# Optimization experiments

Hardware: AMD Instinct MI355X
Metric: run time of the kernel (lower is better)

Reference implementation:

```python
import jax, jax.numpy as jnp
import numpy as np

N, E, C, L, OUT = 50000, 600000, 128, 2, 64


def setup_inputs() -> dict:
    key = jax.random.key(0)
    ks = jax.random.split(key, 8)
    s = 1.0 / np.sqrt(C)
    return {
        "x": jax.random.normal(ks[0], (N, C), jnp.float32),
        "edge_index": jax.random.randint(ks[1], (2, E), 0, N, jnp.int64),
        "W_neigh": jax.random.normal(ks[2], (L, C, C), jnp.float32) * s,
        "W_root": jax.random.normal(ks[3], (L, C, C), jnp.float32) * s,
        "b_conv": jnp.zeros((L, C), jnp.float32),
        "ln_gamma": jnp.ones((L, C), jnp.float32),
        "ln_beta": jnp.zeros((L, C), jnp.float32),
        "W_head": jax.random.normal(ks[4], (OUT, C), jnp.float32) * s,
        "b_head": jnp.zeros((OUT,), jnp.float32),
        "num_seed": 1024,
    }


def _layernorm(h, g, b, eps=1e-5):
    mu = jnp.mean(h, axis=-1, keepdims=True)
    var = jnp.mean(jnp.square(h - mu), axis=-1, keepdims=True)
    return (h - mu) * jax.lax.rsqrt(var + eps) * g + b


def reference(x, edge_index, W_neigh, W_root, b_conv, ln_gamma, ln_beta, W_head, b_head, num_seed):
    src, dst = edge_index[0], edge_index[1]
    n = x.shape[0]
    # in-degree for mean aggregation (clamped to 1 as in PyG mean aggr)
    deg = jax.ops.segment_sum(jnp.ones((src.shape[0],), x.dtype), dst, num_segments=n)
    inv_deg = 1.0 / jnp.maximum(deg, 1.0)  # [N]
    for l in range(W_neigh.shape[0]):
        agg = jax.ops.segment_sum(x[src], dst, num_segments=n) * inv_deg[:, None]  # [N,C]
        h = agg @ W_neigh[l].T + x @ W_root[l].T + b_conv[l]
        x = jax.nn.relu(_layernorm(h, ln_gamma[l], ln_beta[l]))
    # head on the seed nodes (entity table slice starts at 0 here)
    return x[:num_seed] @ W_head.T + b_head
```

## Files before the change

### kernel.cpp

```cpp
#include <hip/hip_runtime.h>

#define C 128

typedef __attribute__((ext_vector_type(8))) short short8;
typedef __attribute__((ext_vector_type(16))) float floatx16;

__device__ __forceinline__ unsigned short f2b(float f) {
    union { float f; unsigned u; } v; v.f = f;
    unsigned u = v.u + 0x7fffu + ((v.u >> 16) & 1u);
    return (unsigned short)(u >> 16);
}
__device__ __forceinline__ float b2f(unsigned short h) {
    union { unsigned u; float f; } v; v.u = ((unsigned)h) << 16;
    return v.f;
}
__device__ __forceinline__ void acc_pair(unsigned u, float& lo, float& hi) {
    union { unsigned u; float f; } a, b;
    a.u = u << 16;
    b.u = u & 0xffff0000u;
    lo += a.f;
    hi += b.f;
}

__global__ void mark_kernel(const int* __restrict__ src, const int* __restrict__ dst,
                            int* __restrict__ needed, int E, int num_seed) {
    int t = blockIdx.x * blockDim.x + threadIdx.x;
    if (t < num_seed) needed[t] = 1;
    if (t < E) {
        int d = dst[t];
        if (d < num_seed) needed[src[t]] = 1;
    }
}

__global__ void cast_count_kernel(const float* __restrict__ x, unsigned short* __restrict__ xb, int n4x,
                                  const float* __restrict__ Wn, unsigned short* __restrict__ Wnb,
                                  const float* __restrict__ Wr, unsigned short* __restrict__ Wrb, int n4w,
                                  const float* __restrict__ Wh, unsigned short* __restrict__ Whb, int n4h,
                                  const int* __restrict__ dst, int* __restrict__ deg, int E,
                                  const int* __restrict__ needed,
                                  int castBlocks) {
    if ((int)blockIdx.x < castBlocks) {
        int i = blockIdx.x * blockDim.x + threadIdx.x;
        const float* in;
        unsigned short* out;
        int idx;
        if (i < n4x) { in = x; out = xb; idx = i; }
        else if (i < n4x + n4w) { in = Wn; out = Wnb; idx = i - n4x; }
        else if (i < n4x + 2 * n4w) { in = Wr; out = Wrb; idx = i - n4x - n4w; }
        else if (i < n4x + 2 * n4w + n4h) { in = Wh; out = Whb; idx = i - n4x - 2 * n4w; }
        else return;
        float4 v = ((const float4*)in)[idx];
        ushort4 o;
        o.x = f2b(v.x); o.y = f2b(v.y); o.z = f2b(v.z); o.w = f2b(v.w);
        ((ushort4*)out)[idx] = o;
    } else {
        int e = (blockIdx.x - castBlocks) * blockDim.x + threadIdx.x;
        if (e < E) {
            int d = dst[e];
            if (!needed || needed[d]) atomicAdd(&deg[d], 1);
        }
    }
}

__global__ void scan_partial2_kernel(const int* __restrict__ deg, const int* __restrict__ needed,
                                     int* __restrict__ bsumD, int* __restrict__ bsumN, int n) {
    __shared__ int smD[256];
    __shared__ int smN[256];
    int t = threadIdx.x;
    int i = blockIdx.x * 256 + t;
    smD[t] = (i < n) ? deg[i] : 0;
    smN[t] = (i < n) ? needed[i] : 0;
    __syncthreads();
#pragma unroll
    for (int off = 128; off > 0; off >>= 1) {
        if (t < off) { smD[t] += smD[t + off]; smN[t] += smN[t + off]; }
        __syncthreads();
    }
    if (t == 0) { bsumD[blockIdx.x] = smD[0]; bsumN[blockIdx.x] = smN[0]; }
}

__global__ void scan_scatter2_kernel(const int* __restrict__ deg, const int* __restrict__ needed,
                                     const int* __restrict__ bsumD, const int* __restrict__ bsumN,
                                     int* __restrict__ row_start, int* __restrict__ cursor,
                                     int* __restrict__ nodelist, int* __restrict__ Mptr,
                                     int n) {
    __shared__ int osmD[256];
    __shared__ int osmN[256];
    __shared__ int smD[256];
    __shared__ int smN[256];
    int t = threadIdx.x, bid = blockIdx.x;
    int sD = 0, sN = 0;
    for (int i = t; i < bid; i += 256) { sD += bsumD[i]; sN += bsumN[i]; }
    osmD[t] = sD; osmN[t] = sN;
    __syncthreads();
#pragma unroll
    for (int off = 128; off > 0; off >>= 1) {
        if (t < off) { osmD[t] += osmD[t + off]; osmN[t] += osmN[t + off]; }
        __syncthreads();
    }
    int boffD = osmD[0], boffN = osmN[0];
    int i = bid * 256 + t;
    int d = (i < n) ? deg[i] : 0;
    int nd = (i < n) ? needed[i] : 0;
    smD[t] = d; smN[t] = nd;
    __syncthreads();
    for (int off = 1; off < 256; off <<= 1) {
        int vD = (t >= off) ? smD[t - off] : 0;
        int vN = (t >= off) ? smN[t - off] : 0;
        __syncthreads();
        smD[t] += vD; smN[t] += vN;
        __syncthreads();
    }
    int exD = smD[t] - d + boffD;
    int exN = smN[t] - nd + boffN;
    if (i < n) {
        row_start[i] = exD;
        cursor[i] = exD;
        if (nd) nodelist[exN] = i;
        if (i == n - 1) { row_start[n] = exD + d; *Mptr = exN + nd; }
    }
}

__global__ void bucket_kernel(const int* __restrict__ src, const int* __restrict__ dst,
                              int* __restrict__ cursor, int* __restrict__ esrc, int E,
                              const int* __restrict__ needed) {
    int e = blockIdx.x * blockDim.x + threadIdx.x;
    if (e < E) {
        int d = dst[e];
        if (!needed || needed[d]) {
            int p = atomicAdd(&cursor[d], 1);
            esrc[p] = src[e];
        }
    }
}

__global__ void aggregate_kernel(const unsigned short* __restrict__ xb, const int* __restrict__ row_start,
                                 const int* __restrict__ esrc,
                                 unsigned short* __restrict__ agg, int n,
                                 const int* __restrict__ nodelist, const int* __restrict__ Mptr) {
    int wid = (blockIdx.x * blockDim.x + threadIdx.x) >> 6;
    int lane = threadIdx.x & 63;
    int q = lane >> 4, l16 = lane & 15;
    int qb = lane & 48;
    int pos = wid * 4 + q;
    int m = Mptr ? *Mptr : n;
    if (pos >= m) return;
    int node = nodelist ? nodelist[pos] : pos;

    int beg = row_start[node];
    int end = row_start[node + 1];
    size_t choff = (size_t)l16 * 8;

    float a0 = 0.f, a1 = 0.f, a2 = 0.f, a3 = 0.f, a4 = 0.f, a5 = 0.f, a6 = 0.f, a7 = 0.f;

    for (int base = beg; base < end; base += 16) {
        int cnt = min(end - base, 16);
        int e_val = (base + l16 < end) ? esrc[base + l16] : 0;
        int j = 0;
        for (; j + 4 <= cnt; j += 4) {
            int s0 = __shfl(e_val, qb | j, 64);
            int s1 = __shfl(e_val, qb | (j + 1), 64);
            int s2 = __shfl(e_val, qb | (j + 2), 64);
            int s3 = __shfl(e_val, qb | (j + 3), 64);
            uint4 v0 = *(const uint4*)(xb + (size_t)s0 * C + choff);
            uint4 v1 = *(const uint4*)(xb + (size_t)s1 * C + choff);
            uint4 v2 = *(const uint4*)(xb + (size_t)s2 * C + choff);
            uint4 v3 = *(const uint4*)(xb + (size_t)s3 * C + choff);
            acc_pair(v0.x, a0, a1); acc_pair(v0.y, a2, a3); acc_pair(v0.z, a4, a5); acc_pair(v0.w, a6, a7);
            acc_pair(v1.x, a0, a1); acc_pair(v1.y, a2, a3); acc_pair(v1.z, a4, a5); acc_pair(v1.w, a6, a7);
            acc_pair(v2.x, a0, a1); acc_pair(v2.y, a2, a3); acc_pair(v2.z, a4, a5); acc_pair(v2.w, a6, a7);
            acc_pair(v3.x, a0, a1); acc_pair(v3.y, a2, a3); acc_pair(v3.z, a4, a5); acc_pair(v3.w, a6, a7);
        }
        for (; j < cnt; ++j) {
            int s0 = __shfl(e_val, qb | j, 64);
            uint4 v0 = *(const uint4*)(xb + (size_t)s0 * C + choff);
            acc_pair(v0.x, a0, a1); acc_pair(v0.y, a2, a3); acc_pair(v0.z, a4, a5); acc_pair(v0.w, a6, a7);
        }
    }

    float sc = 1.0f / fmaxf((float)(end - beg), 1.0f);
    uint4 o;
    o.x = ((unsigned)f2b(a1 * sc) << 16) | (unsigned)f2b(a0 * sc);
    o.y = ((unsigned)f2b(a3 * sc) << 16) | (unsigned)f2b(a2 * sc);
    o.z = ((unsigned)f2b(a5 * sc) << 16) | (unsigned)f2b(a4 * sc);
    o.w = ((unsigned)f2b(a7 * sc) << 16) | (unsigned)f2b(a6 * sc);
    *(uint4*)(agg + (size_t)pos * C + choff) = o;
}

__launch_bounds__(256)
__global__ void gemm_mfma_ln_relu_kernel(const unsigned short* __restrict__ Aagg,
                                         const unsigned short* __restrict__ Xin,
                                         const unsigned short* __restrict__ Wn,
                                         const unsigned short* __restrict__ Wr,
                                         const float* __restrict__ bconv, const float* __restrict__ gamma,
                                         const float* __restrict__ beta, unsigned short* __restrict__ Xout,
                                         int n,
                                         const int* __restrict__ nodelist, const int* __restrict__ Mptr,
                                         const unsigned short* __restrict__ Whb,
                                         const float* __restrict__ bh, float* __restrict__ out) {
    __shared__ unsigned short Xs[64][136];
    __shared__ unsigned short Ws[128][136];
    __shared__ float Ls[64][2];
    __shared__ float Lss[64][2];

    int m = Mptr ? *Mptr : n;
    int row0 = blockIdx.x * 64;
    if (row0 >= m) return;

    int tid = threadIdx.x;
    int wave = tid >> 6, lane = tid & 63;
    int rh = wave & 1, ch = wave >> 1;
    int l31 = lane & 31, half = lane >> 5;

    floatx16 acc0, acc1;
#pragma unroll
    for (int i = 0; i < 16; ++i) { acc0[i] = 0.f; acc1[i] = 0.f; }

#pragma unroll
    for (int phase = 0; phase < 2; ++phase) {
        const unsigned short* Ap = phase ? Xin : Aagg;
        const unsigned short* Wp = phase ? Wr : Wn;
        __syncthreads();
#pragma unroll
        for (int i = 0; i < 4; ++i) {
            int cidx = tid + 256 * i;
            int r = cidx >> 4, koff = (cidx & 15) * 8;
            uint4 v = make_uint4(0u, 0u, 0u, 0u);
            int rg = row0 + r;
            if (rg < m) {
                int rowid = (phase && nodelist) ? nodelist[rg] : rg;
                v = *(const uint4*)(Ap + (size_t)rowid * C + koff);
            }
            *(uint4*)&Xs[r][koff] = v;
        }
#pragma unroll
        for (int i = 0; i < 8; ++i) {
            int cidx = tid + 256 * i;
            int r = cidx >> 4, koff = (cidx & 15) * 8;
            uint4 v = *(const uint4*)(Wp + (size_t)r * C + koff);
            *(uint4*)&Ws[r][koff] = v;
        }
        __syncthreads();
#pragma unroll
        for (int kc = 0; kc < C; kc += 16) {
            int ko = kc + half * 8;
            short8 a = *(const short8*)&Xs[rh * 32 + l31][ko];
            short8 b0 = *(const short8*)&Ws[ch * 64 + l31][ko];
            short8 b1 = *(const short8*)&Ws[ch * 64 + 32 + l31][ko];
            acc0 = __builtin_amdgcn_mfma_f32_32x32x16_bf16(a, b0, acc0, 0, 0, 0);
            acc1 = __builtin_amdgcn_mfma_f32_32x32x16_bf16(a, b1, acc1, 0, 0, 0);
        }
    }

    int col0 = ch * 64 + l31;
    int col1 = col0 + 32;
    float bc0 = bconv[col0], bc1 = bconv[col1];
#pragma unroll
    for (int r = 0; r < 16; ++r) {
        float h0 = acc0[r] + bc0;
        float h1 = acc1[r] + bc1;
        float s = h0 + h1, ss = h0 * h0 + h1 * h1;
#pragma unroll
        for (int mk = 1; mk < 32; mk <<= 1) {
            s += __shfl_xor(s, mk, 64);
            ss += __shfl_xor(ss, mk, 64);
        }
        if (l31 == 0) {
            int row_l = rh * 32 + (r & 3) + 8 * (r >> 2) + 4 * half;
            Ls[row_l][ch] = s;
            Lss[row_l][ch] = ss;
        }
    }
    __syncthreads();

    if (Whb) {
#pragma unroll
        for (int i = 0; i < 4; ++i) {
            int cidx = tid + 256 * i;
            int r = cidx >> 4, koff = (cidx & 15) * 8;
            uint4 v = *(const uint4*)(Whb + (size_t)r * C + koff);
            *(uint4*)&Ws[r][koff] = v;
        }
    }

    float g0 = gamma[col0], g1 = gamma[col1];
    float be0 = beta[col0], be1 = beta[col1];
#pragma unroll
    for (int r = 0; r < 16; ++r) {
        int row_l = rh * 32 + (r & 3) + 8 * (r >> 2) + 4 * half;
        int rg = row0 + row_l;
        float s = Ls[row_l][0] + Ls[row_l][1];
        float ss = Lss[row_l][0] + Lss[row_l][1];
        float mu = s * (1.0f / 128.0f);
        float var = ss * (1.0f / 128.0f) - mu * mu;
        float rs = rsqrtf(var + 1e-5f);
        float h0 = acc0[r] + bc0;
        float h1 = acc1[r] + bc1;
        float o0 = fmaxf((h0 - mu) * rs * g0 + be0, 0.f);
        float o1 = fmaxf((h1 - mu) * rs * g1 + be1, 0.f);
        if (Whb) {
            Xs[row_l][col0] = f2b(o0);
            Xs[row_l][col1] = f2b(o1);
        } else if (rg < m) {
            int orow = nodelist ? nodelist[rg] : rg;
            Xout[(size_t)orow * C + col0] = f2b(o0);
            Xout[(size_t)orow * C + col1] = f2b(o1);
        }
    }

    if (Whb) {
        __syncthreads();
        floatx16 hc;
#pragma unroll
        for (int i = 0; i < 16; ++i) hc[i] = 0.f;
        int m0 = rh * 32, n0 = ch * 32;
#pragma unroll
        for (int kc = 0; kc < C; kc += 16) {
            int ko = kc + half * 8;
            short8 a = *(const short8*)&Xs[m0 + l31][ko];
            short8 b = *(const short8*)&Ws[n0 + l31][ko];
            hc = __builtin_amdgcn_mfma_f32_32x32x16_bf16(a, b, hc, 0, 0, 0);
        }
        int oc = n0 + l31;
        float bhv = bh[oc];
#pragma unroll
        for (int r = 0; r < 16; ++r) {
            int row_l = m0 + (r & 3) + 8 * (r >> 2) + 4 * half;
            int rg = row0 + row_l;
            if (rg < m) out[(size_t)rg * 64 + oc] = hc[r] + bhv;
        }
    }
}

extern "C" void kernel_launch(void* const* d_in, const int* in_sizes, int n_in,
                              void* d_out, int out_size, void* d_ws, size_t ws_size,
                              hipStream_t stream) {
    const float* x = (const float*)d_in[0];
    const int* ei = (const int*)d_in[1];
    const float* Wn = (const float*)d_in[2];
    const float* Wr = (const float*)d_in[3];
    const float* bconv = (const float*)d_in[4];
    const float* gamma = (const float*)d_in[5];
    const float* beta = (const float*)d_in[6];
    const float* Wh = (const float*)d_in[7];
    const float* bh = (const float*)d_in[8];

    int N = in_sizes[0] / C;
    int E = in_sizes[1] / 2;
    int L = in_sizes[2] / (C * C);
    int num_seed = out_size / 64;
    int nchunks = (N + 255) / 256;

    char* ws = (char*)d_ws;
    size_t off = 0;
    auto alloc = [&](size_t bytes) {
        void* p = ws + off;
        off = (off + bytes + 255) & ~(size_t)255;
        return p;
    };
    int* degneed = (int*)alloc((size_t)2 * N * 4);
    int* deg = degneed;
    int* needed = degneed + N;
    int* row_start = (int*)alloc((size_t)(N + 1) * 4);
    int* cursor = (int*)alloc((size_t)N * 4);
    int* nodelist = (int*)alloc((size_t)N * 4);
    int* Mptr = (int*)alloc(4);
    int* bsumD = (int*)alloc((size_t)nchunks * 4);
    int* bsumN = (int*)alloc((size_t)nchunks * 4);
    int* esrc = (int*)alloc((size_t)E * 4);
    unsigned short* xb = (unsigned short*)alloc((size_t)N * C * 2);
    unsigned short* aggb = (unsigned short*)alloc((size_t)N * C * 2);
    unsigned short* xA = (unsigned short*)alloc((size_t)N * C * 2);
    unsigned short* xB = (unsigned short*)alloc((size_t)N * C * 2);
    unsigned short* Wnb = (unsigned short*)alloc((size_t)L * C * C * 2);
    unsigned short* Wrb = (unsigned short*)alloc((size_t)L * C * C * 2);
    unsigned short* Whb = (unsigned short*)alloc((size_t)64 * C * 2);

    const int* srcIdx = ei;
    const int* dstIdx = ei + E;

    int n4x = N * C / 4;
    int n4w = L * C * C / 4;
    int n4h = 64 * C / 4;
    int castBlocks = (n4x + 2 * n4w + n4h + 255) / 256;
    int degBlocks = (E + 255) / 256;

    const int* filt = (L == 2) ? needed : nullptr;

    hipMemsetAsync(degneed, 0, (size_t)2 * N * 4, stream);
    int markBlocks = (max(E, num_seed) + 255) / 256;
    mark_kernel<<<markBlocks, 256, 0, stream>>>(srcIdx, dstIdx, needed, E, num_seed);
    cast_count_kernel<<<castBlocks + degBlocks, 256, 0, stream>>>(
        x, xb, n4x, Wn, Wnb, Wr, Wrb, n4w, Wh, Whb, n4h, dstIdx, deg, E, filt, castBlocks);
    scan_partial2_kernel<<<nchunks, 256, 0, stream>>>(deg, needed, bsumD, bsumN, N);
    scan_scatter2_kernel<<<nchunks, 256, 0, stream>>>(deg, needed, bsumD, bsumN,
                                                      row_start, cursor, nodelist, Mptr, N);
    bucket_kernel<<<degBlocks, 256, 0, stream>>>(srcIdx, dstIdx, cursor, esrc, E, filt);

    const unsigned short* cur = xb;
    unsigned short* bufs[2] = {xA, xB};
    for (int l = 0; l < L; ++l) {
        bool last = (l == L - 1);
        bool front = !last && (l == L - 2);
        int nl = last ? num_seed : N;
        const int* list = front ? nodelist : nullptr;
        const int* Mp = front ? Mptr : nullptr;
        unsigned short* nxt = bufs[l & 1];
        int aggThreads = ((nl + 3) / 4) * 64;
        aggregate_kernel<<<(aggThreads + 255) / 256, 256, 0, stream>>>(
            cur, row_start, esrc, aggb, nl, list, Mp);
        gemm_mfma_ln_relu_kernel<<<(nl + 63) / 64, 256, 0, stream>>>(
            aggb, cur, Wnb + (size_t)l * C * C, Wrb + (size_t)l * C * C,
            bconv + (size_t)l * C, gamma + (size_t)l * C, beta + (size_t)l * C, nxt, nl,
            list, Mp,
            last ? Whb : (const unsigned short*)nullptr, bh, (float*)d_out);
        cur = nxt;
    }
}
```

Baseline: 166.0 us.

## Fuse neighbor aggregation into GEMM and merge preprocessing kernels with lookback scan

Folds the per-layer mean-aggregation gather into the MFMA GEMM+LayerNorm kernel, so each block gathers its 64 rows straight into shared memory instead of writing and re-reading a bf16 aggregate buffer. The gather loop is also unrolled to eight neighbors per step. The separate mark kernel is merged into the cast/degree kernel, and the two-pass block scan is replaced by a single-pass decoupled-lookback scan. Together these cut kernel launches and global memory traffic. In exchange, degree counting now runs over all edges unfiltered, and the fused kernel has to hide gather latency with fewer waves because of its large shared-memory footprint.

```diff
diff --git a/kernel.cpp b/kernel.cpp
--- a/kernel.cpp
+++ b/kernel.cpp
@@ -9,10 +9,6 @@
     union { float f; unsigned u; } v; v.f = f;
     unsigned u = v.u + 0x7fffu + ((v.u >> 16) & 1u);
     return (unsigned short)(u >> 16);
-}
-__device__ __forceinline__ float b2f(unsigned short h) {
-    union { unsigned u; float f; } v; v.u = ((unsigned)h) << 16;
-    return v.f;
 }
 __device__ __forceinline__ void acc_pair(unsigned u, float& lo, float& hi) {
     union { unsigned u; float f; } a, b;
@@ -22,23 +18,14 @@
     hi += b.f;
 }
 
-__global__ void mark_kernel(const int* __restrict__ src, const int* __restrict__ dst,
-                            int* __restrict__ needed, int E, int num_seed) {
-    int t = blockIdx.x * blockDim.x + threadIdx.x;
-    if (t < num_seed) needed[t] = 1;
-    if (t < E) {
-        int d = dst[t];
-        if (d < num_seed) needed[src[t]] = 1;
-    }
-}
-
-__global__ void cast_count_kernel(const float* __restrict__ x, unsigned short* __restrict__ xb, int n4x,
-                                  const float* __restrict__ Wn, unsigned short* __restrict__ Wnb,
-                                  const float* __restrict__ Wr, unsigned short* __restrict__ Wrb, int n4w,
-                                  const float* __restrict__ Wh, unsigned short* __restrict__ Whb, int n4h,
-                                  const int* __restrict__ dst, int* __restrict__ deg, int E,
-                                  const int* __restrict__ needed,
-                                  int castBlocks) {
+__global__ void cast_mark_count_kernel(const float* __restrict__ x, unsigned short* __restrict__ xb, int n4x,
+                                       const float* __restrict__ Wn, unsigned short* __restrict__ Wnb,
+                                       const float* __restrict__ Wr, unsigned short* __restrict__ Wrb, int n4w,
+                                       const float* __restrict__ Wh, unsigned short* __restrict__ Whb, int n4h,
+                                       const int* __restrict__ src, const int* __restrict__ dst,
+                                       int* __restrict__ deg, int* __restrict__ needed,
+                                       int E, int num_seed,
+                                       int castBlocks) {
     if ((int)blockIdx.x < castBlocks) {
         int i = blockIdx.x * blockDim.x + threadIdx.x;
         const float* in;
@@ -55,50 +42,26 @@
         ((ushort4*)out)[idx] = o;
     } else {
         int e = (blockIdx.x - castBlocks) * blockDim.x + threadIdx.x;
+        if (e < num_seed) needed[e] = 1;
         if (e < E) {
             int d = dst[e];
-            if (!needed || needed[d]) atomicAdd(&deg[d], 1);
-        }
-    }
-}
-
-__global__ void scan_partial2_kernel(const int* __restrict__ deg, const int* __restrict__ needed,
-                                     int* __restrict__ bsumD, int* __restrict__ bsumN, int n) {
+            atomicAdd(&deg[d], 1);
+            if (d < num_seed) needed[src[e]] = 1;
+        }
+    }
+}
+
+__global__ void scan_fused_kernel(const int* __restrict__ deg, const int* __restrict__ needed,
+                                  unsigned long long* __restrict__ status, int* __restrict__ counter,
+                                  int* __restrict__ row_start, int* __restrict__ cursor,
+                                  int* __restrict__ nodelist, int* __restrict__ Mptr, int n) {
     __shared__ int smD[256];
     __shared__ int smN[256];
+    __shared__ int sbid, sprefD, sprefN;
     int t = threadIdx.x;
-    int i = blockIdx.x * 256 + t;
-    smD[t] = (i < n) ? deg[i] : 0;
-    smN[t] = (i < n) ? needed[i] : 0;
-    __syncthreads();
-#pragma unroll
-    for (int off = 128; off > 0; off >>= 1) {
-        if (t < off) { smD[t] += smD[t + off]; smN[t] += smN[t + off]; }
-        __syncthreads();
-    }
-    if (t == 0) { bsumD[blockIdx.x] = smD[0]; bsumN[blockIdx.x] = smN[0]; }
-}
-
-__global__ void scan_scatter2_kernel(const int* __restrict__ deg, const int* __restrict__ needed,
-                                     const int* __restrict__ bsumD, const int* __restrict__ bsumN,
-                                     int* __restrict__ row_start, int* __restrict__ cursor,
-                                     int* __restrict__ nodelist, int* __restrict__ Mptr,
-                                     int n) {
-    __shared__ int osmD[256];
-    __shared__ int osmN[256];
-    __shared__ int smD[256];
-    __shared__ int smN[256];
-    int t = threadIdx.x, bid = blockIdx.x;
-    int sD = 0, sN = 0;
-    for (int i = t; i < bid; i += 256) { sD += bsumD[i]; sN += bsumN[i]; }
-    osmD[t] = sD; osmN[t] = sN;
-    __syncthreads();
-#pragma unroll
-    for (int off = 128; off > 0; off >>= 1) {
-        if (t < off) { osmD[t] += osmD[t + off]; osmN[t] += osmN[t + off]; }
-        __syncthreads();
-    }
-    int boffD = osmD[0], boffN = osmN[0];
+    if (t == 0) sbid = atomicAdd(counter, 1);
+    __syncthreads();
+    int bid = sbid;
     int i = bid * 256 + t;
     int d = (i < n) ? deg[i] : 0;
     int nd = (i < n) ? needed[i] : 0;
@@ -111,8 +74,34 @@
         smD[t] += vD; smN[t] += vN;
         __syncthreads();
     }
-    int exD = smD[t] - d + boffD;
-    int exN = smN[t] - nd + boffN;
+    int totD = smD[255], totN = smN[255];
+    if (t == 0) {
+        if (bid == 0) {
+            atomicExch(&status[0],
+                       (2ULL << 62) | ((unsigned long long)(unsigned)totN << 32) | (unsigned)totD);
+            sprefD = 0; sprefN = 0;
+        } else {
+            atomicExch(&status[bid],
+                       (1ULL << 62) | ((unsigned long long)(unsigned)totN << 32) | (unsigned)totD);
+            int accD = 0, accN = 0;
+            for (int j = bid - 1; j >= 0;) {
+                unsigned long long v = atomicAdd(&status[j], 0ULL);
+                unsigned f = (unsigned)(v >> 62);
+                if (f == 0) { __builtin_amdgcn_s_sleep(1); continue; }
+                accD += (int)(unsigned)(v & 0xffffffffULL);
+                accN += (int)((v >> 32) & 0x3fffffffULL);
+                if (f == 2) break;
+                --j;
+            }
+            atomicExch(&status[bid],
+                       (2ULL << 62) | ((unsigned long long)(unsigned)(accN + totN) << 32) |
+                           (unsigned)(accD + totD));
+            sprefD = accD; sprefN = accN;
+        }
+    }
+    __syncthreads();
+    int exD = smD[t] - d + sprefD;
+    int exN = smN[t] - nd + sprefN;
     if (i < n) {
         row_start[i] = exD;
         cursor[i] = exD;
@@ -127,77 +116,24 @@
     int e = blockIdx.x * blockDim.x + threadIdx.x;
     if (e < E) {
         int d = dst[e];
-        if (!needed || needed[d]) {
+        if (needed[d]) {
             int p = atomicAdd(&cursor[d], 1);
             esrc[p] = src[e];
         }
     }
 }
 
-__global__ void aggregate_kernel(const unsigned short* __restrict__ xb, const int* __restrict__ row_start,
-                                 const int* __restrict__ esrc,
-                                 unsigned short* __restrict__ agg, int n,
-                                 const int* __restrict__ nodelist, const int* __restrict__ Mptr) {
-    int wid = (blockIdx.x * blockDim.x + threadIdx.x) >> 6;
-    int lane = threadIdx.x & 63;
-    int q = lane >> 4, l16 = lane & 15;
-    int qb = lane & 48;
-    int pos = wid * 4 + q;
-    int m = Mptr ? *Mptr : n;
-    if (pos >= m) return;
-    int node = nodelist ? nodelist[pos] : pos;
-
-    int beg = row_start[node];
-    int end = row_start[node + 1];
-    size_t choff = (size_t)l16 * 8;
-
-    float a0 = 0.f, a1 = 0.f, a2 = 0.f, a3 = 0.f, a4 = 0.f, a5 = 0.f, a6 = 0.f, a7 = 0.f;
-
-    for (int base = beg; base < end; base += 16) {
-        int cnt = min(end - base, 16);
-        int e_val = (base + l16 < end) ? esrc[base + l16] : 0;
-        int j = 0;
-        for (; j + 4 <= cnt; j += 4) {
-            int s0 = __shfl(e_val, qb | j, 64);
-            int s1 = __shfl(e_val, qb | (j + 1), 64);
-            int s2 = __shfl(e_val, qb | (j + 2), 64);
-            int s3 = __shfl(e_val, qb | (j + 3), 64);
-            uint4 v0 = *(const uint4*)(xb + (size_t)s0 * C + choff);
-            uint4 v1 = *(const uint4*)(xb + (size_t)s1 * C + choff);
-            uint4 v2 = *(const uint4*)(xb + (size_t)s2 * C + choff);
-            uint4 v3 = *(const uint4*)(xb + (size_t)s3 * C + choff);
-            acc_pair(v0.x, a0, a1); acc_pair(v0.y, a2, a3); acc_pair(v0.z, a4, a5); acc_pair(v0.w, a6, a7);
-            acc_pair(v1.x, a0, a1); acc_pair(v1.y, a2, a3); acc_pair(v1.z, a4, a5); acc_pair(v1.w, a6, a7);
-            acc_pair(v2.x, a0, a1); acc_pair(v2.y, a2, a3); acc_pair(v2.z, a4, a5); acc_pair(v2.w, a6, a7);
-            acc_pair(v3.x, a0, a1); acc_pair(v3.y, a2, a3); acc_pair(v3.z, a4, a5); acc_pair(v3.w, a6, a7);
-        }
-        for (; j < cnt; ++j) {
-            int s0 = __shfl(e_val, qb | j, 64);
-            uint4 v0 = *(const uint4*)(xb + (size_t)s0 * C + choff);
-            acc_pair(v0.x, a0, a1); acc_pair(v0.y, a2, a3); acc_pair(v0.z, a4, a5); acc_pair(v0.w, a6, a7);
-        }
-    }
-
-    float sc = 1.0f / fmaxf((float)(end - beg), 1.0f);
-    uint4 o;
-    o.x = ((unsigned)f2b(a1 * sc) << 16) | (unsigned)f2b(a0 * sc);
-    o.y = ((unsigned)f2b(a3 * sc) << 16) | (unsigned)f2b(a2 * sc);
-    o.z = ((unsigned)f2b(a5 * sc) << 16) | (unsigned)f2b(a4 * sc);
-    o.w = ((unsigned)f2b(a7 * sc) << 16) | (unsigned)f2b(a6 * sc);
-    *(uint4*)(agg + (size_t)pos * C + choff) = o;
-}
-
 __launch_bounds__(256)
-__global__ void gemm_mfma_ln_relu_kernel(const unsigned short* __restrict__ Aagg,
-                                         const unsigned short* __restrict__ Xin,
-                                         const unsigned short* __restrict__ Wn,
-                                         const unsigned short* __restrict__ Wr,
-                                         const float* __restrict__ bconv, const float* __restrict__ gamma,
-                                         const float* __restrict__ beta, unsigned short* __restrict__ Xout,
-                                         int n,
-                                         const int* __restrict__ nodelist, const int* __restrict__ Mptr,
-                                         const unsigned short* __restrict__ Whb,
-                                         const float* __restrict__ bh, float* __restrict__ out) {
+__global__ void gemm_fused_kernel(const unsigned short* __restrict__ cur,
+                                  const int* __restrict__ row_start, const int* __restrict__ esrc,
+                                  const unsigned short* __restrict__ Wn,
+                                  const unsigned short* __restrict__ Wr,
+                                  const float* __restrict__ bconv, const float* __restrict__ gamma,
+                                  const float* __restrict__ beta, unsigned short* __restrict__ Xout,
+                                  int n,
+                                  const int* __restrict__ nodelist, const int* __restrict__ Mptr,
+                                  const unsigned short* __restrict__ Whb,
+                                  const float* __restrict__ bh, float* __restrict__ out) {
     __shared__ unsigned short Xs[64][136];
     __shared__ unsigned short Ws[128][136];
     __shared__ float Ls[64][2];
@@ -212,44 +148,129 @@
     int rh = wave & 1, ch = wave >> 1;
     int l31 = lane & 31, half = lane >> 5;
 
+#pragma unroll
+    for (int i = 0; i < 8; ++i) {
+        int cidx = tid + 256 * i;
+        int r = cidx >> 4, koff = (cidx & 15) * 8;
+        *(uint4*)&Ws[r][koff] = *(const uint4*)(Wn + (size_t)r * C + koff);
+    }
+
+    int q = lane >> 4, l16 = lane & 15, qb = lane & 48;
+    size_t choff = (size_t)l16 * 8;
+#pragma unroll
+    for (int pass = 0; pass < 4; ++pass) {
+        int rl = pass * 16 + wave * 4 + q;
+        int rg = row0 + rl;
+        float a0 = 0.f, a1 = 0.f, a2 = 0.f, a3 = 0.f, a4 = 0.f, a5 = 0.f, a6 = 0.f, a7 = 0.f;
+        float sc = 0.f;
+        if (rg < m) {
+            int node = nodelist ? nodelist[rg] : rg;
+            int beg = row_start[node];
+            int end = row_start[node + 1];
+            for (int base = beg; base < end; base += 16) {
+                int cnt = min(end - base, 16);
+                int e_val = (base + l16 < end) ? esrc[base + l16] : 0;
+                int j = 0;
+                for (; j + 8 <= cnt; j += 8) {
+                    int s0 = __shfl(e_val, qb | j, 64);
+                    int s1 = __shfl(e_val, qb | (j + 1), 64);
+                    int s2 = __shfl(e_val, qb | (j + 2), 64);
+                    int s3 = __shfl(e_val, qb | (j + 3), 64);
+                    int s4 = __shfl(e_val, qb | (j + 4), 64);
+                    int s5 = __shfl(e_val, qb | (j + 5), 64);
+                    int s6 = __shfl(e_val, qb | (j + 6), 64);
+                    int s7 = __shfl(e_val, qb | (j + 7), 64);
+                    uint4 v0 = *(const uint4*)(cur + (size_t)s0 * C + choff);
+                    uint4 v1 = *(const uint4*)(cur + (size_t)s1 * C + choff);
+                    uint4 v2 = *(const uint4*)(cur + (size_t)s2 * C + choff);
+                    uint4 v3 = *(const uint4*)(cur + (size_t)s3 * C + choff);
+                    uint4 v4 = *(const uint4*)(cur + (size_t)s4 * C + choff);
+                    uint4 v5 = *(const uint4*)(cur + (size_t)s5 * C + choff);
+                    uint4 v6 = *(const uint4*)(cur + (size_t)s6 * C + choff);
+                    uint4 v7 = *(const uint4*)(cur + (size_t)s7 * C + choff);
+                    acc_pair(v0.x, a0, a1); acc_pair(v0.y, a2, a3); acc_pair(v0.z, a4, a5); acc_pair(v0.w, a6, a7);
+                    acc_pair(v1.x, a0, a1); acc_pair(v1.y, a2, a3); acc_pair(v1.z, a4, a5); acc_pair(v1.w, a6, a7);
+                    acc_pair(v2.x, a0, a1); acc_pair(v2.y, a2, a3); acc_pair(v2.z, a4, a5); acc_pair(v2.w, a6, a7);
+                    acc_pair(v3.x, a0, a1); acc_pair(v3.y, a2, a3); acc_pair(v3.z, a4, a5); acc_pair(v3.w, a6, a7);
+                    acc_pair(v4.x, a0, a1); acc_pair(v4.y, a2, a3); acc_pair(v4.z, a4, a5); acc_pair(v4.w, a6, a7);
+                    acc_pair(v5.x, a0, a1); acc_pair(v5.y, a2, a3); acc_pair(v5.z, a4, a5); acc_pair(v5.w, a6, a7);
+                    acc_pair(v6.x, a0, a1); acc_pair(v6.y, a2, a3); acc_pair(v6.z, a4, a5); acc_pair(v6.w, a6, a7);
+                    acc_pair(v7.x, a0, a1); acc_pair(v7.y, a2, a3); acc_pair(v7.z, a4, a5); acc_pair(v7.w, a6, a7);
+                }
+                for (; j + 4 <= cnt; j += 4) {
+                    int s0 = __shfl(e_val, qb | j, 64);
+                    int s1 = __shfl(e_val, qb | (j + 1), 64);
+                    int s2 = __shfl(e_val, qb | (j + 2), 64);
+                    int s3 = __shfl(e_val, qb | (j + 3), 64);
+                    uint4 v0 = *(const uint4*)(cur + (size_t)s0 * C + choff);
+                    uint4 v1 = *(const uint4*)(cur + (size_t)s1 * C + choff);
+                    uint4 v2 = *(const uint4*)(cur + (size_t)s2 * C + choff);
+                    uint4 v3 = *(const uint4*)(cur + (size_t)s3 * C + choff);
+                    acc_pair(v0.x, a0, a1); acc_pair(v0.y, a2, a3); acc_pair(v0.z, a4, a5); acc_pair(v0.w, a6, a7);
+                    acc_pair(v1.x, a0, a1); acc_pair(v1.y, a2, a3); acc_pair(v1.z, a4, a5); acc_pair(v1.w, a6, a7);
+                    acc_pair(v2.x, a0, a1); acc_pair(v2.y, a2, a3); acc_pair(v2.z, a4, a5); acc_pair(v2.w, a6, a7);
+                    acc_pair(v3.x, a0, a1); acc_pair(v3.y, a2, a3); acc_pair(v3.z, a4, a5); acc_pair(v3.w, a6, a7);
+                }
+                for (; j < cnt; ++j) {
+                    int s0 = __shfl(e_val, qb | j, 64);
+                    uint4 v0 = *(const uint4*)(cur + (size_t)s0 * C + choff);
+                    acc_pair(v0.x, a0, a1); acc_pair(v0.y, a2, a3); acc_pair(v0.z, a4, a5); acc_pair(v0.w, a6, a7);
+                }
+            }
+            sc = 1.0f / fmaxf((float)(end - beg), 1.0f);
+        }
+        uint4 o;
+        o.x = ((unsigned)f2b(a1 * sc) << 16) | (unsigned)f2b(a0 * sc);
+        o.y = ((unsigned)f2b(a3 * sc) << 16) | (unsigned)f2b(a2 * sc);
+        o.z = ((unsigned)f2b(a5 * sc) << 16) | (unsigned)f2b(a4 * sc);
+        o.w = ((unsigned)f2b(a7 * sc) << 16) | (unsigned)f2b(a6 * sc);
+        *(uint4*)&Xs[rl][choff] = o;
+    }
+    __syncthreads();
+
     floatx16 acc0, acc1;
 #pragma unroll
     for (int i = 0; i < 16; ++i) { acc0[i] = 0.f; acc1[i] = 0.f; }
 
 #pragma unroll
-    for (int phase = 0; phase < 2; ++phase) {
-        const unsigned short* Ap = phase ? Xin : Aagg;
-        const unsigned short* Wp = phase ? Wr : Wn;
-        __syncthreads();
-#pragma unroll
-        for (int i = 0; i < 4; ++i) {
-            int cidx = tid + 256 * i;
-            int r = cidx >> 4, koff = (cidx & 15) * 8;
-            uint4 v = make_uint4(0u, 0u, 0u, 0u);
-            int rg = row0 + r;
-            if (rg < m) {
-                int rowid = (phase && nodelist) ? nodelist[rg] : rg;
-                v = *(const uint4*)(Ap + (size_t)rowid * C + koff);
-            }
-            *(uint4*)&Xs[r][koff] = v;
-        }
-#pragma unroll
-        for (int i = 0; i < 8; ++i) {
-            int cidx = tid + 256 * i;
-            int r = cidx >> 4, koff = (cidx & 15) * 8;
-            uint4 v = *(const uint4*)(Wp + (size_t)r * C + koff);
-            *(uint4*)&Ws[r][koff] = v;
-        }
-        __syncthreads();
-#pragma unroll
-        for (int kc = 0; kc < C; kc += 16) {
-            int ko = kc + half * 8;
-            short8 a = *(const short8*)&Xs[rh * 32 + l31][ko];
-            short8 b0 = *(const short8*)&Ws[ch * 64 + l31][ko];
-            short8 b1 = *(const short8*)&Ws[ch * 64 + 32 + l31][ko];
-            acc0 = __builtin_amdgcn_mfma_f32_32x32x16_bf16(a, b0, acc0, 0, 0, 0);
-            acc1 = __builtin_amdgcn_mfma_f32_32x32x16_bf16(a, b1, acc1, 0, 0, 0);
-        }
+    for (int kc = 0; kc < C; kc += 16) {
+        int ko = kc + half * 8;
+        short8 a = *(const short8*)&Xs[rh * 32 + l31][ko];
+        short8 b0 = *(const short8*)&Ws[ch * 64 + l31][ko];
+        short8 b1 = *(const short8*)&Ws[ch * 64 + 32 + l31][ko];
+        acc0 = __builtin_amdgcn_mfma_f32_32x32x16_bf16(a, b0, acc0, 0, 0, 0);
+        acc1 = __builtin_amdgcn_mfma_f32_32x32x16_bf16(a, b1, acc1, 0, 0, 0);
+    }
+    __syncthreads();
+
+#pragma unroll
+    for (int i = 0; i < 4; ++i) {
+        int cidx = tid + 256 * i;
+        int r = cidx >> 4, koff = (cidx & 15) * 8;
+        uint4 v = make_uint4(0u, 0u, 0u, 0u);
+        int rg = row0 + r;
+        if (rg < m) {
+            int rowid = nodelist ? nodelist[rg] : rg;
+            v = *(const uint4*)(cur + (size_t)rowid * C + koff);
+        }
+        *(uint4*)&Xs[r][koff] = v;
+    }
+#pragma unroll
+    for (int i = 0; i < 8; ++i) {
+        int cidx = tid + 256 * i;
+        int r = cidx >> 4, koff = (cidx & 15) * 8;
+        *(uint4*)&Ws[r][koff] = *(const uint4*)(Wr + (size_t)r * C + koff);
+    }
+    __syncthreads();
+
+#pragma unroll
+    for (int kc = 0; kc < C; kc += 16) {
+        int ko = kc + half * 8;
+        short8 a = *(const short8*)&Xs[rh * 32 + l31][ko];
+        short8 b0 = *(const short8*)&Ws[ch * 64 + l31][ko];
+        short8 b1 = *(const short8*)&Ws[ch * 64 + 32 + l31][ko];
+        acc0 = __builtin_amdgcn_mfma_f32_32x32x16_bf16(a, b0, acc0, 0, 0, 0);
+        acc1 = __builtin_amdgcn_mfma_f32_32x32x16_bf16(a, b1, acc1, 0, 0, 0);
     }
 
     int col0 = ch * 64 + l31;
@@ -358,18 +379,17 @@
         off = (off + bytes + 255) & ~(size_t)255;
         return p;
     };
-    int* degneed = (int*)alloc((size_t)2 * N * 4);
-    int* deg = degneed;
-    int* needed = degneed + N;
+    int* deg = (int*)alloc((size_t)N * 4);
+    int* needed = (int*)alloc((size_t)N * 4);
+    int* counter = (int*)alloc(256);
+    unsigned long long* status = (unsigned long long*)alloc((size_t)nchunks * 8);
+    size_t zero_span = off;
     int* row_start = (int*)alloc((size_t)(N + 1) * 4);
     int* cursor = (int*)alloc((size_t)N * 4);
     int* nodelist = (int*)alloc((size_t)N * 4);
     int* Mptr = (int*)alloc(4);
-    int* bsumD = (int*)alloc((size_t)nchunks * 4);
-    int* bsumN = (int*)alloc((size_t)nchunks * 4);
     int* esrc = (int*)alloc((size_t)E * 4);
     unsigned short* xb = (unsigned short*)alloc((size_t)N * C * 2);
-    unsigned short* aggb = (unsigned short*)alloc((size_t)N * C * 2);
     unsigned short* xA = (unsigned short*)alloc((size_t)N * C * 2);
     unsigned short* xB = (unsigned short*)alloc((size_t)N * C * 2);
     unsigned short* Wnb = (unsigned short*)alloc((size_t)L * C * C * 2);
@@ -383,19 +403,15 @@
     int n4w = L * C * C / 4;
     int n4h = 64 * C / 4;
     int castBlocks = (n4x + 2 * n4w + n4h + 255) / 256;
-    int degBlocks = (E + 255) / 256;
-
-    const int* filt = (L == 2) ? needed : nullptr;
-
-    hipMemsetAsync(degneed, 0, (size_t)2 * N * 4, stream);
-    int markBlocks = (max(E, num_seed) + 255) / 256;
-    mark_kernel<<<markBlocks, 256, 0, stream>>>(srcIdx, dstIdx, needed, E, num_seed);
-    cast_count_kernel<<<castBlocks + degBlocks, 256, 0, stream>>>(
-        x, xb, n4x, Wn, Wnb, Wr, Wrb, n4w, Wh, Whb, n4h, dstIdx, deg, E, filt, castBlocks);
-    scan_partial2_kernel<<<nchunks, 256, 0, stream>>>(deg, needed, bsumD, bsumN, N);
-    scan_scatter2_kernel<<<nchunks, 256, 0, stream>>>(deg, needed, bsumD, bsumN,
-                                                      row_start, cursor, nodelist, Mptr, N);
-    bucket_kernel<<<degBlocks, 256, 0, stream>>>(srcIdx, dstIdx, cursor, esrc, E, filt);
+    int degBlocks = (max(E, num_seed) + 255) / 256;
+
+    hipMemsetAsync(ws, 0, zero_span, stream);
+    cast_mark_count_kernel<<<castBlocks + degBlocks, 256, 0, stream>>>(
+        x, xb, n4x, Wn, Wnb, Wr, Wrb, n4w, Wh, Whb, n4h,
+        srcIdx, dstIdx, deg, needed, E, num_seed, castBlocks);
+    scan_fused_kernel<<<nchunks, 256, 0, stream>>>(deg, needed, status, counter,
+                                                   row_start, cursor, nodelist, Mptr, N);
+    bucket_kernel<<<(E + 255) / 256, 256, 0, stream>>>(srcIdx, dstIdx, cursor, esrc, E, needed);
 
     const unsigned short* cur = xb;
     unsigned short* bufs[2] = {xA, xB};
@@ -406,11 +422,9 @@
         const int* list = front ? nodelist : nullptr;
         const int* Mp = front ? Mptr : nullptr;
         unsigned short* nxt = bufs[l & 1];
-        int aggThreads = ((nl + 3) / 4) * 64;
-        aggregate_kernel<<<(aggThreads + 255) / 256, 256, 0, stream>>>(
-            cur, row_start, esrc, aggb, nl, list, Mp);
-        gemm_mfma_ln_relu_kernel<<<(nl + 63) / 64, 256, 0, stream>>>(
-            aggb, cur, Wnb + (size_t)l * C * C, Wrb + (size_t)l * C * C,
+        gemm_fused_kernel<<<(nl + 63) / 64, 256, 0, stream>>>(
+            cur, row_start, esrc,
+            Wnb + (size_t)l * C * C, Wrb + (size_t)l * C * C,
             bconv + (size_t)l * C, gamma + (size_t)l * C, beta + (size_t)l * C, nxt, nl,
             list, Mp,
             last ? Whb : (const unsigned short*)nullptr, bh, (float*)d_out);
```

After: 197.9 us. 1.19x slower.
